# Performance work log

Hardware: AMD Instinct MI355X
Metric: run time of the kernel (lower is better)

The kernel has to match this reference:

```python
import jax, jax.numpy as jnp
import numpy as np

MODEL_DIM = 2048
INNER_DIM = 512
NUM_HEADS = 16
FFN_DIM = 8192
MEM_TOKENS = 64
BATCH = 2
SEQ = 2048
EPS = 1e-6


def _rmsnorm(x, w):
    # norm = ||x|| / sqrt(d); out = w * x / (norm + eps)
    norm = jnp.linalg.norm(x, axis=-1, keepdims=True) / np.sqrt(x.shape[-1])
    return w * x / (norm + EPS)


def setup_inputs() -> dict:
    key = jax.random.key(0)
    names_shapes = [
        ("x", (BATCH, SEQ, MODEL_DIM)), ("memory", (BATCH, MEM_TOKENS, MODEL_DIM)),
        ("wq", (MODEL_DIM, MODEL_DIM)), ("wk", (MODEL_DIM, MODEL_DIM)),
        ("wv", (MODEL_DIM, MODEL_DIM)), ("wz", (MODEL_DIM, MODEL_DIM)),
        ("wg", (MODEL_DIM, MODEL_DIM)),
        ("md1", (MODEL_DIM, INNER_DIM)), ("md2", (INNER_DIM, MODEL_DIM)),
        ("mcw", (MODEL_DIM, MODEL_DIM)),
        ("awq", (MODEL_DIM, MODEL_DIM)), ("awk", (MODEL_DIM, MODEL_DIM)),
        ("awv", (MODEL_DIM, MODEL_DIM)), ("awo", (MODEL_DIM, MODEL_DIM)),
        ("f1", (MODEL_DIM, FFN_DIM)), ("f2", (FFN_DIM, MODEL_DIM)),
    ]
    keys = jax.random.split(key, len(names_shapes))
    inp = {}
    for (name, shape), k in zip(names_shapes, keys):
        scale = 1.0 if name in ("x", "memory") else 0.02
        inp[name] = jax.random.normal(k, shape, dtype=jnp.float32) * scale
    for name, dim in [("bq", MODEL_DIM), ("bk", MODEL_DIM), ("bv", MODEL_DIM),
                      ("bz", MODEL_DIM), ("bg", MODEL_DIM), ("mb1", INNER_DIM),
                      ("mb2", MODEL_DIM), ("mcb", MODEL_DIM), ("abq", MODEL_DIM),
                      ("abk", MODEL_DIM), ("abv", MODEL_DIM), ("abo", MODEL_DIM),
                      ("fb1", FFN_DIM), ("fb2", MODEL_DIM)]:
        inp[name] = jnp.zeros((dim,), dtype=jnp.float32)
    inp["n1w"] = jnp.ones((MODEL_DIM,), dtype=jnp.float32)
    inp["n2w"] = jnp.ones((MODEL_DIM,), dtype=jnp.float32)
    return inp


def reference(x, memory, wq, bq, wk, bk, wv, bv, wz, bz, wg, bg, n1w, n2w,
              md1, mb1, md2, mb2, mcw, mcb, awq, abq, awk, abk, awv, abv,
              awo, abo, f1, fb1, f2, fb2):
    B, S, D = x.shape
    H = NUM_HEADS
    dh = D // H

    # 1. projections on RMS-normed input
    xn = _rmsnorm(x, n1w)
    k_ = xn @ wk + bk
    v_ = xn @ wv + bv  # computed as in original (feeds attention path via h_t)
    z = xn @ wz + bz

    # MDI decay gamma: 2-layer decay net + context modulation, sigmoid
    gamma = jax.nn.sigmoid((jax.nn.gelu(z @ md1 + mb1) @ md2 + mb2)
                           + (k_ @ mcw + mcb))

    # 2. associative scan (exponential cumulative product) on contiguous reshape
    g4 = gamma.reshape(B, H, S, dh)  # faithful torch .view semantics
    cumprod = jnp.cumprod(g4, axis=2).reshape(B, S, D)

    # 3-4. core formula: h_t = z_t * sigmoid(W_g h_prev) + gamma * h_prev
    gate = jax.nn.sigmoid(x @ wg + bg)
    h_t = z * gate + gamma * x

    # 5. multi-memory attention: queries from h_t, keys/values from memory bank
    qa = (h_t @ awq + abq).reshape(B, S, H, dh)
    ka = (memory @ awk + abk).reshape(B, -1, H, dh)
    va = (memory @ awv + abv).reshape(B, -1, H, dh)
    scores = jnp.einsum('bshd,bmhd->bhsm', qa, ka) / np.sqrt(dh)
    attn = jax.nn.softmax(scores, axis=-1)
    ctx = jnp.einsum('bhsm,bmhd->bshd', attn, va).reshape(B, S, D)
    mem_context = ctx @ awo + abo

    # 6. residuals (dropout in eval mode = identity)
    x_residual = x + (h_t + mem_context)

    # 7. FFN + residual
    xn2 = _rmsnorm(x_residual, n2w)
    ffn_out = jax.nn.gelu(xn2 @ f1 + fb1) @ f2 + fb2
    output = x_residual + ffn_out
    return output, cumprod
```

## Files before the change

### kernel.cpp

```cpp
#include <hip/hip_runtime.h>
#include <stdint.h>
#include <stddef.h>


#define DEV __device__ __forceinline__

typedef __attribute__((ext_vector_type(8))) short bh8;
typedef __attribute__((ext_vector_type(4))) float f32x4;

typedef __attribute__((address_space(1))) uint32_t gu32;
typedef __attribute__((address_space(3))) uint32_t lu32;

DEV void async16(const void* g, void* l) {
  __builtin_amdgcn_global_load_lds((gu32*)g, (lu32*)l, 16, 0, 0);
}

DEV float b2f(short s) {
  union { float f; uint32_t u; } x;
  x.u = ((uint32_t)(uint16_t)s) << 16;
  return x.f;
}
DEV short f2b(float f) {
  uint32_t u = __float_as_uint(f);
  u += 0x7fffu + ((u >> 16) & 1u);
  return (short)(u >> 16);
}
DEV float sigmoid_f(float x) { return 1.f / (1.f + __expf(-x)); }
DEV float gelu_f(float x) {
  float y = 0.7978845608028654f * (x + 0.044715f * x * x * x);
  float t = 1.f - 2.f / (__expf(2.f * y) + 1.f);
  return 0.5f * x * (1.f + t);
}

template <int EPI>
DEV void epi_store(float v, size_t idx, void* Cv, const void* aux0, const void* aux1) {
  if constexpr (EPI == 0) {
    ((short*)Cv)[idx] = f2b(v);
  } else if constexpr (EPI == 1) {
    ((short*)Cv)[idx] = f2b(gelu_f(v));
  } else if constexpr (EPI == 2) {
    ((float*)Cv)[idx] = v;
  } else if constexpr (EPI == 3) {
    ((float*)Cv)[idx] = sigmoid_f(v + ((const float*)aux0)[idx]);
  } else if constexpr (EPI == 4) {
    ((float*)Cv)[idx] = v + ((const float*)aux0)[idx] + b2f(((const short*)aux1)[idx]);
  } else {
    ((float*)Cv)[idx] = v + ((const float*)aux0)[idx];
  }
}

template <int EPI>
__global__ __launch_bounds__(512) void gemm8_k(
    const short* __restrict__ A, const short* __restrict__ Bt,
    const float* __restrict__ bias, void* Cv,
    const void* aux0, const void* aux1, int M, int N, int K) {
  __shared__ __align__(16) short sL[3 * 24576];
  const int tid  = threadIdx.x;
  const int lane = tid & 63;
  const int wave = tid >> 6;
  const int q = lane >> 4;
  const int r = lane & 15;
  const int wm = wave >> 2;
  const int wn = wave & 3;

  const int nwg = gridDim.x * gridDim.y;
  int flat = blockIdx.y * gridDim.x + blockIdx.x;
  flat = (flat & 7) * (nwg >> 3) + (flat >> 3);
  const int bx = flat % gridDim.x;
  const int by = flat / gridDim.x;
  const int m0 = by * 128;
  const int n0 = bx * 256;

  const int srow = tid >> 3;
  const int sk8  = (tid & 7) ^ (srow & 7);
  const short* pA = A  + (size_t)(m0 + srow) * K + sk8 * 8;
  const short* pB = Bt + (size_t)(n0 + srow) * K + sk8 * 8;
  const size_t K64 = (size_t)64 * K;
  short* dA = &sL[tid * 8];
  short* dB = &sL[8192 + tid * 8];

#define STAGE_B(bi, t) do {                        \
    const short* s_ = pB + (size_t)(t) * 64;       \
    short* d_ = dB + (bi) * 24576;                 \
    async16(s_,           d_);                     \
    async16(s_ + K64,     d_ + 4096);              \
    async16(s_ + 2 * K64, d_ + 8192);              \
    async16(s_ + 3 * K64, d_ + 12288);             \
  } while (0)
#define STAGE_A(bi, t) do {                        \
    const short* s_ = pA + (size_t)(t) * 64;       \
    short* d_ = dA + (bi) * 24576;                 \
    async16(s_,       d_);                         \
    async16(s_ + K64, d_ + 4096);                  \
  } while (0)

  const int swz0 = (q ^ (r & 7)) * 8;
  const int swz1 = ((4 + q) ^ (r & 7)) * 8;
  const int aRow = (wm * 64 + r) * 64;
  const int bRow = 8192 + (wn * 64 + r) * 64;

  f32x4 acc[4][4] = {};
  const int NT = K >> 6;

  STAGE_B(0, 0); STAGE_A(0, 0);
  if (NT > 1) {
    STAGE_B(1, 1); STAGE_A(1, 1);
    asm volatile("s_waitcnt vmcnt(6)" ::: "memory");
  } else {
    asm volatile("s_waitcnt vmcnt(0)" ::: "memory");
  }
  __builtin_amdgcn_s_barrier();

  int cb = 0;
  for (int t = 0; t < NT; ++t) {
    const short* buf = &sL[cb * 24576];
    bh8 af[4][2], bf[4][2];
#pragma unroll
    for (int i = 0; i < 4; ++i) {
      af[i][0] = *(const bh8*)&buf[aRow + i * 1024 + swz0];
      af[i][1] = *(const bh8*)&buf[aRow + i * 1024 + swz1];
    }
#pragma unroll
    for (int j = 0; j < 4; ++j) {
      bf[j][0] = *(const bh8*)&buf[bRow + j * 1024 + swz0];
      bf[j][1] = *(const bh8*)&buf[bRow + j * 1024 + swz1];
    }
    if (t + 2 < NT) {
      const int pb = (cb == 0) ? 2 : cb - 1;
      STAGE_B(pb, t + 2);
      STAGE_A(pb, t + 2);
    }
#pragma unroll
    for (int kk = 0; kk < 2; ++kk)
#pragma unroll
      for (int i = 0; i < 4; ++i)
#pragma unroll
        for (int j = 0; j < 4; ++j)
          acc[i][j] = __builtin_amdgcn_mfma_f32_16x16x32_bf16(
              af[i][kk], bf[j][kk], acc[i][j], 0, 0, 0);
    if (t + 2 < NT) asm volatile("s_waitcnt vmcnt(6)" ::: "memory");
    else            asm volatile("s_waitcnt vmcnt(0)" ::: "memory");
    __builtin_amdgcn_s_barrier();
    cb = (cb == 2) ? 0 : cb + 1;
  }
#undef STAGE_A
#undef STAGE_B

#pragma unroll
  for (int j = 0; j < 4; ++j) {
    const int col = n0 + wn * 64 + j * 16 + r;
    const float bv = bias[col];
#pragma unroll
    for (int i = 0; i < 4; ++i) {
#pragma unroll
      for (int rr = 0; rr < 4; ++rr) {
        const int row = m0 + wm * 64 + i * 16 + q * 4 + rr;
        const size_t idx = (size_t)row * N + col;
        epi_store<EPI>(acc[i][j][rr] + bv, idx, Cv, aux0, aux1);
      }
    }
  }
}

__global__ __launch_bounds__(256) void transpose_k(const float* __restrict__ in,
                                                   short* __restrict__ out,
                                                   int R, int C) {
  __shared__ float t[64][68];
  const int tx = threadIdx.x, ty = threadIdx.y;
  const int c0 = blockIdx.x * 64, r0 = blockIdx.y * 64;
#pragma unroll
  for (int yy = 0; yy < 64; yy += 16) {
    const float4 v = *(const float4*)&in[(size_t)(r0 + ty + yy) * C + c0 + tx * 4];
    t[ty + yy][tx * 4 + 0] = v.x;
    t[ty + yy][tx * 4 + 1] = v.y;
    t[ty + yy][tx * 4 + 2] = v.z;
    t[ty + yy][tx * 4 + 3] = v.w;
  }
  __syncthreads();
#pragma unroll
  for (int yy = 0; yy < 64; yy += 16) {
    short4 v;
    v.x = f2b(t[tx * 4 + 0][ty + yy]);
    v.y = f2b(t[tx * 4 + 1][ty + yy]);
    v.z = f2b(t[tx * 4 + 2][ty + yy]);
    v.w = f2b(t[tx * 4 + 3][ty + yy]);
    *(short4*)&out[(size_t)(c0 + ty + yy) * R + r0 + tx * 4] = v;
  }
}

__global__ __launch_bounds__(256) void cvt_k(const float* __restrict__ in,
                                             short* __restrict__ out) {
  const size_t i = ((size_t)blockIdx.x * 256 + threadIdx.x) * 4;
  const float4 v = *(const float4*)(in + i);
  short4 o;
  o.x = f2b(v.x); o.y = f2b(v.y); o.z = f2b(v.z); o.w = f2b(v.w);
  *(short4*)(out + i) = o;
}

__global__ __launch_bounds__(256) void rmsnorm_k(const float* __restrict__ in,
                                                 const float* __restrict__ w,
                                                 short* __restrict__ out) {
  const int row = blockIdx.x;
  const int tid = threadIdx.x;
  const size_t base = (size_t)row * 2048;
  float v[8];
  const float* p = in + base + tid * 8;
#pragma unroll
  for (int i = 0; i < 8; ++i) v[i] = p[i];
  float ss = 0.f;
#pragma unroll
  for (int i = 0; i < 8; ++i) ss += v[i] * v[i];
  for (int off = 32; off; off >>= 1) ss += __shfl_down(ss, off);
  __shared__ float red[4];
  __shared__ float sscale;
  if ((tid & 63) == 0) red[tid >> 6] = ss;
  __syncthreads();
  if (tid == 0) {
    float tot = red[0] + red[1] + red[2] + red[3];
    sscale = 1.f / (sqrtf(tot * (1.f / 2048.f)) + 1e-6f);
  }
  __syncthreads();
  const float scale = sscale;
  short* o = out + base + tid * 8;
#pragma unroll
  for (int i = 0; i < 8; ++i) o[i] = f2b(w[tid * 8 + i] * v[i] * scale);
}

__global__ __launch_bounds__(256) void ht_k(const short* __restrict__ z,
                                            const short* __restrict__ gp,
                                            const float* __restrict__ gamma,
                                            const float* __restrict__ x,
                                            short* __restrict__ ht) {
  const size_t i = ((size_t)blockIdx.x * 256 + threadIdx.x) * 4;
  const short4 z4 = *(const short4*)(z + i);
  const short4 g4 = *(const short4*)(gp + i);
  const float4 x4 = *(const float4*)(x + i);
  const float4 gm = *(const float4*)(gamma + i);
  short4 o;
  o.x = f2b(b2f(z4.x) * sigmoid_f(b2f(g4.x)) + gm.x * x4.x);
  o.y = f2b(b2f(z4.y) * sigmoid_f(b2f(g4.y)) + gm.y * x4.y);
  o.z = f2b(b2f(z4.z) * sigmoid_f(b2f(g4.z)) + gm.z * x4.z);
  o.w = f2b(b2f(z4.w) * sigmoid_f(b2f(g4.w)) + gm.w * x4.w);
  *(short4*)(ht + i) = o;
}

__global__ __launch_bounds__(128) void cumprod1_k(float* __restrict__ gamma,
                                                  float* __restrict__ segprod) {
  const int bx = blockIdx.x;
  const int b = bx >> 7, h = (bx >> 3) & 15, seg = bx & 7;
  size_t base = (size_t)b * 4194304 + (size_t)h * 262144 + (size_t)seg * 256 * 128 + threadIdx.x;
  float acc = 1.f;
  for (int s = 0; s < 256; ++s) {
    acc *= gamma[base + (size_t)s * 128];
    gamma[base + (size_t)s * 128] = acc;
  }
  segprod[(size_t)bx * 128 + threadIdx.x] = acc;
}

__global__ __launch_bounds__(128) void cumprod2_k(const float* __restrict__ gamma,
                                                  const float* __restrict__ segprod,
                                                  float* __restrict__ out) {
  const int bx = blockIdx.x;
  const int b = bx >> 7, h = (bx >> 3) & 15, seg = bx & 7;
  size_t base = (size_t)b * 4194304 + (size_t)h * 262144 + (size_t)seg * 256 * 128 + threadIdx.x;
  float pre = 1.f;
  const size_t sp0 = (size_t)(bx & ~7) * 128 + threadIdx.x;
  for (int t = 0; t < seg; ++t) pre *= segprod[sp0 + (size_t)t * 128];
  for (int s = 0; s < 256; ++s)
    out[base + (size_t)s * 128] = gamma[base + (size_t)s * 128] * pre;
}

__global__ __launch_bounds__(512) void attn_k(const short* __restrict__ qa,
                                              const short* __restrict__ ka,
                                              const short* __restrict__ va,
                                              short* __restrict__ ctx) {
  __shared__ short sk[64][136];
  __shared__ short sv[64][136];
  __shared__ float sq[32][128];
  __shared__ float ss[32][64];
  const int tid = threadIdx.x;
  const int b = blockIdx.z, h = blockIdx.y;
  const int s0 = blockIdx.x * 32;
  const size_t hoff = (size_t)h * 128;
  for (int i = tid; i < 64 * 128; i += 512) {
    int m = i >> 7, d = i & 127;
    sk[m][d] = ka[((size_t)b * 64 + m) * 2048 + hoff + d];
    sv[m][d] = va[((size_t)b * 64 + m) * 2048 + hoff + d];
  }
  for (int i = tid; i < 32 * 128; i += 512) {
    int s = i >> 7, d = i & 127;
    sq[s][d] = b2f(qa[((size_t)b * 2048 + s0 + s) * 2048 + hoff + d]);
  }
  __syncthreads();
  const int g = tid >> 4;
  const int t = tid & 15;
  float sc[4];
#pragma unroll
  for (int mi = 0; mi < 4; ++mi) {
    const int m = mi * 16 + t;
    float a = 0.f;
    for (int d = 0; d < 128; ++d) a += sq[g][d] * b2f(sk[m][d]);
    sc[mi] = a * 0.08838834764831843f;
  }
  float mx = fmaxf(fmaxf(sc[0], sc[1]), fmaxf(sc[2], sc[3]));
#pragma unroll
  for (int off = 8; off; off >>= 1) mx = fmaxf(mx, __shfl_xor(mx, off, 16));
  float sum = 0.f;
#pragma unroll
  for (int mi = 0; mi < 4; ++mi) { sc[mi] = __expf(sc[mi] - mx); sum += sc[mi]; }
#pragma unroll
  for (int off = 8; off; off >>= 1) sum += __shfl_xor(sum, off, 16);
  const float inv = 1.f / sum;
#pragma unroll
  for (int mi = 0; mi < 4; ++mi) ss[g][mi * 16 + t] = sc[mi] * inv;
  __syncthreads();
  const int d0 = t * 8;
  float o[8] = {};
  for (int m = 0; m < 64; ++m) {
    const float wgt = ss[g][m];
#pragma unroll
    for (int i = 0; i < 8; ++i) o[i] += wgt * b2f(sv[m][d0 + i]);
  }
  short* op = ctx + ((size_t)b * 2048 + s0 + g) * 2048 + hoff + d0;
#pragma unroll
  for (int i = 0; i < 8; ++i) op[i] = f2b(o[i]);
}

extern "C" void kernel_launch(void* const* d_in, const int* in_sizes, int n_in,
                              void* d_out, int out_size, void* d_ws, size_t ws_size,
                              hipStream_t stream) {
  (void)in_sizes; (void)n_in; (void)out_size; (void)ws_size;
  const float* x   = (const float*)d_in[0];
  const float* mem = (const float*)d_in[1];
  const float* wk  = (const float*)d_in[3];
  const float* wz  = (const float*)d_in[5];
  const float* wg  = (const float*)d_in[6];
  const float* md1 = (const float*)d_in[7];
  const float* md2 = (const float*)d_in[8];
  const float* mcw = (const float*)d_in[9];
  const float* awq = (const float*)d_in[10];
  const float* awk = (const float*)d_in[11];
  const float* awv = (const float*)d_in[12];
  const float* awo = (const float*)d_in[13];
  const float* f1  = (const float*)d_in[14];
  const float* f2  = (const float*)d_in[15];
  const float* bk  = (const float*)d_in[17];
  const float* bz  = (const float*)d_in[19];
  const float* bg  = (const float*)d_in[20];
  const float* mb1 = (const float*)d_in[21];
  const float* mb2 = (const float*)d_in[22];
  const float* mcb = (const float*)d_in[23];
  const float* abq = (const float*)d_in[24];
  const float* abk = (const float*)d_in[25];
  const float* abv = (const float*)d_in[26];
  const float* abo = (const float*)d_in[27];
  const float* fb1 = (const float*)d_in[28];
  const float* fb2 = (const float*)d_in[29];
  const float* n1w = (const float*)d_in[30];
  const float* n2w = (const float*)d_in[31];

  char* W = (char*)d_ws;
  short* wkT  = (short*)(W + 0);
  short* wzT  = (short*)(W + 8388608);
  short* wgT  = (short*)(W + 16777216);
  short* mcwT = (short*)(W + 25165824);
  short* md1T = (short*)(W + 33554432);
  short* md2T = (short*)(W + 35651584);
  short* awqT = (short*)(W + 37748736);
  short* awkT = (short*)(W + 46137344);
  short* awvT = (short*)(W + 54525952);
  short* awoT = (short*)(W + 62914560);
  short* f1T  = (short*)(W + 71303168);
  short* f2T  = (short*)(W + 104857600);
  char*  big  = W + 138412032;
  short* xn   = (short*)(big + 0);
  short* kk   = (short*)(big + 16777216);
  short* z    = (short*)(big + 33554432);
  short* gpre = (short*)(big + 50331648);
  short* ctx  = kk;
  short* t2   = (short*)big;
  short* t1   = (short*)(W + 205520896);
  float* gamma = (float*)(W + 209715200);
  float* xres  = gamma;
  short* ht   = (short*)(W + 243269632);
  short* qa   = (short*)(W + 260046848);
  short* xn2  = qa;
  short* xb   = (short*)(W + 276824064);
  short* memb = (short*)(W + 293601280);
  short* ka   = (short*)(W + 294125568);
  short* va   = (short*)(W + 294649856);
  float* segprod = (float*)(W + 295174144);

  float* out0 = (float*)d_out;
  float* out1 = out0 + 8388608;

  const dim3 tb16(16, 16);
  transpose_k<<<dim3(32, 32), tb16, 0, stream>>>(wk, wkT, 2048, 2048);
  transpose_k<<<dim3(32, 32), tb16, 0, stream>>>(wz, wzT, 2048, 2048);
  transpose_k<<<dim3(32, 32), tb16, 0, stream>>>(wg, wgT, 2048, 2048);
  transpose_k<<<dim3(32, 32), tb16, 0, stream>>>(mcw, mcwT, 2048, 2048);
  transpose_k<<<dim3(8, 32), tb16, 0, stream>>>(md1, md1T, 2048, 512);
  transpose_k<<<dim3(32, 8), tb16, 0, stream>>>(md2, md2T, 512, 2048);
  transpose_k<<<dim3(32, 32), tb16, 0, stream>>>(awq, awqT, 2048, 2048);
  transpose_k<<<dim3(32, 32), tb16, 0, stream>>>(awk, awkT, 2048, 2048);
  transpose_k<<<dim3(32, 32), tb16, 0, stream>>>(awv, awvT, 2048, 2048);
  transpose_k<<<dim3(32, 32), tb16, 0, stream>>>(awo, awoT, 2048, 2048);
  transpose_k<<<dim3(128, 32), tb16, 0, stream>>>(f1, f1T, 2048, 8192);
  transpose_k<<<dim3(32, 128), tb16, 0, stream>>>(f2, f2T, 8192, 2048);

  cvt_k<<<8192, 256, 0, stream>>>(x, xb);
  cvt_k<<<256, 256, 0, stream>>>(mem, memb);
  rmsnorm_k<<<4096, 256, 0, stream>>>(x, n1w, xn);

  gemm8_k<0><<<dim3(8, 32), 512, 0, stream>>>(xn, wkT, bk, kk, nullptr, nullptr, 4096, 2048, 2048);
  gemm8_k<0><<<dim3(8, 32), 512, 0, stream>>>(xn, wzT, bz, z, nullptr, nullptr, 4096, 2048, 2048);
  gemm8_k<0><<<dim3(8, 32), 512, 0, stream>>>(xb, wgT, bg, gpre, nullptr, nullptr, 4096, 2048, 2048);

  gemm8_k<1><<<dim3(2, 32), 512, 0, stream>>>(z, md1T, mb1, t1, nullptr, nullptr, 4096, 512, 2048);
  gemm8_k<2><<<dim3(8, 32), 512, 0, stream>>>(t1, md2T, mb2, gamma, nullptr, nullptr, 4096, 2048, 512);
  gemm8_k<3><<<dim3(8, 32), 512, 0, stream>>>(kk, mcwT, mcb, gamma, gamma, nullptr, 4096, 2048, 2048);

  ht_k<<<8192, 256, 0, stream>>>(z, gpre, gamma, x, ht);

  cumprod1_k<<<256, 128, 0, stream>>>(gamma, segprod);
  cumprod2_k<<<256, 128, 0, stream>>>(gamma, segprod, out1);

  gemm8_k<0><<<dim3(8, 32), 512, 0, stream>>>(ht, awqT, abq, qa, nullptr, nullptr, 4096, 2048, 2048);
  gemm8_k<0><<<dim3(8, 1), 512, 0, stream>>>(memb, awkT, abk, ka, nullptr, nullptr, 128, 2048, 2048);
  gemm8_k<0><<<dim3(8, 1), 512, 0, stream>>>(memb, awvT, abv, va, nullptr, nullptr, 128, 2048, 2048);

  attn_k<<<dim3(64, 16, 2), 512, 0, stream>>>(qa, ka, va, ctx);

  gemm8_k<4><<<dim3(8, 32), 512, 0, stream>>>(ctx, awoT, abo, xres, x, ht, 4096, 2048, 2048);

  rmsnorm_k<<<4096, 256, 0, stream>>>(xres, n2w, xn2);

  gemm8_k<1><<<dim3(32, 32), 512, 0, stream>>>(xn2, f1T, fb1, t2, nullptr, nullptr, 4096, 8192, 2048);
  gemm8_k<5><<<dim3(8, 32), 512, 0, stream>>>(t2, f2T, fb2, out0, xres, nullptr, 4096, 2048, 8192);
}
```

Before: 1.207 ms.

## Split GEMM k-step into barrier-separated halves and fuse h_t and x casts

The GEMM main loop is split into two half-k phases. Each phase loads its LDS fragments, issues part of the next prefetch, synchronises with a barrier and raises wave priority around its MFMA block, aiming to overlap LDS reads, global prefetch and matrix work across waves. The separate h_t elementwise kernel is folded into the gamma GEMM epilogue (new EPI 6), which writes h_t at a fixed offset from the gamma buffer. The bf16 cast of x is folded into the first RMSNorm kernel. Together these cut kernel launches and memory round-trips, at the cost of extra barriers per k-step and a hardcoded buffer-adjacency assumption for h_t.

```diff
diff --git a/kernel.cpp b/kernel.cpp
--- a/kernel.cpp
+++ b/kernel.cpp
@@ -33,7 +33,8 @@
 }
 
 template <int EPI>
-DEV void epi_store(float v, size_t idx, void* Cv, const void* aux0, const void* aux1) {
+DEV void epi_store(float v, size_t idx, void* Cv, const void* aux0,
+                   const void* aux1, const void* aux2, const void* aux3) {
   if constexpr (EPI == 0) {
     ((short*)Cv)[idx] = f2b(v);
   } else if constexpr (EPI == 1) {
@@ -44,8 +45,16 @@
     ((float*)Cv)[idx] = sigmoid_f(v + ((const float*)aux0)[idx]);
   } else if constexpr (EPI == 4) {
     ((float*)Cv)[idx] = v + ((const float*)aux0)[idx] + b2f(((const short*)aux1)[idx]);
+  } else if constexpr (EPI == 5) {
+    ((float*)Cv)[idx] = v + ((const float*)aux0)[idx];
   } else {
-    ((float*)Cv)[idx] = v + ((const float*)aux0)[idx];
+    const float g = sigmoid_f(v + ((const float*)aux0)[idx]);
+    ((float*)Cv)[idx] = g;
+    const float xv = ((const float*)aux1)[idx];
+    const float zz = b2f(((const short*)aux2)[idx]);
+    const float gp = b2f(((const short*)aux3)[idx]);
+    short* ht = (short*)((float*)Cv + 8388608);
+    ht[idx] = f2b(zz * sigmoid_f(gp) + g * xv);
   }
 }
 
@@ -53,7 +62,8 @@
 __global__ __launch_bounds__(512) void gemm8_k(
     const short* __restrict__ A, const short* __restrict__ Bt,
     const float* __restrict__ bias, void* Cv,
-    const void* aux0, const void* aux1, int M, int N, int K) {
+    const void* aux0, const void* aux1, const void* aux2, const void* aux3,
+    int M, int N, int K) {
   __shared__ __align__(16) short sL[3 * 24576];
   const int tid  = threadIdx.x;
   const int lane = tid & 63;
@@ -103,43 +113,55 @@
   const int NT = K >> 6;
 
   STAGE_B(0, 0); STAGE_A(0, 0);
-  if (NT > 1) {
-    STAGE_B(1, 1); STAGE_A(1, 1);
-    asm volatile("s_waitcnt vmcnt(6)" ::: "memory");
-  } else {
-    asm volatile("s_waitcnt vmcnt(0)" ::: "memory");
-  }
+  STAGE_B(1, 1); STAGE_A(1, 1);
+  asm volatile("s_waitcnt vmcnt(6)" ::: "memory");
   __builtin_amdgcn_s_barrier();
 
   int cb = 0;
   for (int t = 0; t < NT; ++t) {
     const short* buf = &sL[cb * 24576];
-    bh8 af[4][2], bf[4][2];
-#pragma unroll
-    for (int i = 0; i < 4; ++i) {
-      af[i][0] = *(const bh8*)&buf[aRow + i * 1024 + swz0];
-      af[i][1] = *(const bh8*)&buf[aRow + i * 1024 + swz1];
-    }
-#pragma unroll
-    for (int j = 0; j < 4; ++j) {
-      bf[j][0] = *(const bh8*)&buf[bRow + j * 1024 + swz0];
-      bf[j][1] = *(const bh8*)&buf[bRow + j * 1024 + swz1];
-    }
-    if (t + 2 < NT) {
-      const int pb = (cb == 0) ? 2 : cb - 1;
-      STAGE_B(pb, t + 2);
-      STAGE_A(pb, t + 2);
-    }
-#pragma unroll
-    for (int kk = 0; kk < 2; ++kk)
-#pragma unroll
-      for (int i = 0; i < 4; ++i)
-#pragma unroll
-        for (int j = 0; j < 4; ++j)
-          acc[i][j] = __builtin_amdgcn_mfma_f32_16x16x32_bf16(
-              af[i][kk], bf[j][kk], acc[i][j], 0, 0, 0);
-    if (t + 2 < NT) asm volatile("s_waitcnt vmcnt(6)" ::: "memory");
-    else            asm volatile("s_waitcnt vmcnt(0)" ::: "memory");
+    const int pb = (cb == 0) ? 2 : cb - 1;
+    const bool pf = (t + 2 < NT);
+
+    bh8 af0[4], bf0[4];
+#pragma unroll
+    for (int i = 0; i < 4; ++i) af0[i] = *(const bh8*)&buf[aRow + i * 1024 + swz0];
+#pragma unroll
+    for (int j = 0; j < 4; ++j) bf0[j] = *(const bh8*)&buf[bRow + j * 1024 + swz0];
+    if (pf) STAGE_B(pb, t + 2);
+    __builtin_amdgcn_s_barrier();
+    asm volatile("s_waitcnt lgkmcnt(0)" ::: "memory");
+    __builtin_amdgcn_sched_barrier(0);
+    __builtin_amdgcn_s_setprio(1);
+#pragma unroll
+    for (int i = 0; i < 4; ++i)
+#pragma unroll
+      for (int j = 0; j < 4; ++j)
+        acc[i][j] = __builtin_amdgcn_mfma_f32_16x16x32_bf16(
+            af0[i], bf0[j], acc[i][j], 0, 0, 0);
+    __builtin_amdgcn_s_setprio(0);
+    __builtin_amdgcn_s_barrier();
+
+    bh8 af1[4], bf1[4];
+#pragma unroll
+    for (int i = 0; i < 4; ++i) af1[i] = *(const bh8*)&buf[aRow + i * 1024 + swz1];
+#pragma unroll
+    for (int j = 0; j < 4; ++j) bf1[j] = *(const bh8*)&buf[bRow + j * 1024 + swz1];
+    if (pf) STAGE_A(pb, t + 2);
+    __builtin_amdgcn_s_barrier();
+    asm volatile("s_waitcnt lgkmcnt(0)" ::: "memory");
+    __builtin_amdgcn_sched_barrier(0);
+    __builtin_amdgcn_s_setprio(1);
+#pragma unroll
+    for (int i = 0; i < 4; ++i)
+#pragma unroll
+      for (int j = 0; j < 4; ++j)
+        acc[i][j] = __builtin_amdgcn_mfma_f32_16x16x32_bf16(
+            af1[i], bf1[j], acc[i][j], 0, 0, 0);
+    __builtin_amdgcn_s_setprio(0);
+
+    if (pf) asm volatile("s_waitcnt vmcnt(6)" ::: "memory");
+    else    asm volatile("s_waitcnt vmcnt(0)" ::: "memory");
     __builtin_amdgcn_s_barrier();
     cb = (cb == 2) ? 0 : cb + 1;
   }
@@ -156,7 +178,7 @@
       for (int rr = 0; rr < 4; ++rr) {
         const int row = m0 + wm * 64 + i * 16 + q * 4 + rr;
         const size_t idx = (size_t)row * N + col;
-        epi_store<EPI>(acc[i][j][rr] + bv, idx, Cv, aux0, aux1);
+        epi_store<EPI>(acc[i][j][rr] + bv, idx, Cv, aux0, aux1, aux2, aux3);
       }
     }
   }
@@ -199,7 +221,8 @@
 
 __global__ __launch_bounds__(256) void rmsnorm_k(const float* __restrict__ in,
                                                  const float* __restrict__ w,
-                                                 short* __restrict__ out) {
+                                                 short* __restrict__ out,
+                                                 short* __restrict__ xbout) {
   const int row = blockIdx.x;
   const int tid = threadIdx.x;
   const size_t base = (size_t)row * 2048;
@@ -207,6 +230,11 @@
   const float* p = in + base + tid * 8;
 #pragma unroll
   for (int i = 0; i < 8; ++i) v[i] = p[i];
+  if (xbout) {
+    short* xo = xbout + base + tid * 8;
+#pragma unroll
+    for (int i = 0; i < 8; ++i) xo[i] = f2b(v[i]);
+  }
   float ss = 0.f;
 #pragma unroll
   for (int i = 0; i < 8; ++i) ss += v[i] * v[i];
@@ -224,24 +252,6 @@
   short* o = out + base + tid * 8;
 #pragma unroll
   for (int i = 0; i < 8; ++i) o[i] = f2b(w[tid * 8 + i] * v[i] * scale);
-}
-
-__global__ __launch_bounds__(256) void ht_k(const short* __restrict__ z,
-                                            const short* __restrict__ gp,
-                                            const float* __restrict__ gamma,
-                                            const float* __restrict__ x,
-                                            short* __restrict__ ht) {
-  const size_t i = ((size_t)blockIdx.x * 256 + threadIdx.x) * 4;
-  const short4 z4 = *(const short4*)(z + i);
-  const short4 g4 = *(const short4*)(gp + i);
-  const float4 x4 = *(const float4*)(x + i);
-  const float4 gm = *(const float4*)(gamma + i);
-  short4 o;
-  o.x = f2b(b2f(z4.x) * sigmoid_f(b2f(g4.x)) + gm.x * x4.x);
-  o.y = f2b(b2f(z4.y) * sigmoid_f(b2f(g4.y)) + gm.y * x4.y);
-  o.z = f2b(b2f(z4.z) * sigmoid_f(b2f(g4.z)) + gm.z * x4.z);
-  o.w = f2b(b2f(z4.w) * sigmoid_f(b2f(g4.w)) + gm.w * x4.w);
-  *(short4*)(ht + i) = o;
 }
 
 __global__ __launch_bounds__(128) void cumprod1_k(float* __restrict__ gamma,
@@ -408,33 +418,30 @@
   transpose_k<<<dim3(128, 32), tb16, 0, stream>>>(f1, f1T, 2048, 8192);
   transpose_k<<<dim3(32, 128), tb16, 0, stream>>>(f2, f2T, 8192, 2048);
 
-  cvt_k<<<8192, 256, 0, stream>>>(x, xb);
   cvt_k<<<256, 256, 0, stream>>>(mem, memb);
-  rmsnorm_k<<<4096, 256, 0, stream>>>(x, n1w, xn);
-
-  gemm8_k<0><<<dim3(8, 32), 512, 0, stream>>>(xn, wkT, bk, kk, nullptr, nullptr, 4096, 2048, 2048);
-  gemm8_k<0><<<dim3(8, 32), 512, 0, stream>>>(xn, wzT, bz, z, nullptr, nullptr, 4096, 2048, 2048);
-  gemm8_k<0><<<dim3(8, 32), 512, 0, stream>>>(xb, wgT, bg, gpre, nullptr, nullptr, 4096, 2048, 2048);
-
-  gemm8_k<1><<<dim3(2, 32), 512, 0, stream>>>(z, md1T, mb1, t1, nullptr, nullptr, 4096, 512, 2048);
-  gemm8_k<2><<<dim3(8, 32), 512, 0, stream>>>(t1, md2T, mb2, gamma, nullptr, nullptr, 4096, 2048, 512);
-  gemm8_k<3><<<dim3(8, 32), 512, 0, stream>>>(kk, mcwT, mcb, gamma, gamma, nullptr, 4096, 2048, 2048);
-
-  ht_k<<<8192, 256, 0, stream>>>(z, gpre, gamma, x, ht);
+  rmsnorm_k<<<4096, 256, 0, stream>>>(x, n1w, xn, xb);
+
+  gemm8_k<0><<<dim3(8, 32), 512, 0, stream>>>(xn, wkT, bk, kk, nullptr, nullptr, nullptr, nullptr, 4096, 2048, 2048);
+  gemm8_k<0><<<dim3(8, 32), 512, 0, stream>>>(xn, wzT, bz, z, nullptr, nullptr, nullptr, nullptr, 4096, 2048, 2048);
+  gemm8_k<0><<<dim3(8, 32), 512, 0, stream>>>(xb, wgT, bg, gpre, nullptr, nullptr, nullptr, nullptr, 4096, 2048, 2048);
+
+  gemm8_k<1><<<dim3(2, 32), 512, 0, stream>>>(z, md1T, mb1, t1, nullptr, nullptr, nullptr, nullptr, 4096, 512, 2048);
+  gemm8_k<2><<<dim3(8, 32), 512, 0, stream>>>(t1, md2T, mb2, gamma, nullptr, nullptr, nullptr, nullptr, 4096, 2048, 512);
+  gemm8_k<6><<<dim3(8, 32), 512, 0, stream>>>(kk, mcwT, mcb, gamma, gamma, x, z, gpre, 4096, 2048, 2048);
 
   cumprod1_k<<<256, 128, 0, stream>>>(gamma, segprod);
   cumprod2_k<<<256, 128, 0, stream>>>(gamma, segprod, out1);
 
-  gemm8_k<0><<<dim3(8, 32), 512, 0, stream>>>(ht, awqT, abq, qa, nullptr, nullptr, 4096, 2048, 2048);
-  gemm8_k<0><<<dim3(8, 1), 512, 0, stream>>>(memb, awkT, abk, ka, nullptr, nullptr, 128, 2048, 2048);
-  gemm8_k<0><<<dim3(8, 1), 512, 0, stream>>>(memb, awvT, abv, va, nullptr, nullptr, 128, 2048, 2048);
+  gemm8_k<0><<<dim3(8, 32), 512, 0, stream>>>(ht, awqT, abq, qa, nullptr, nullptr, nullptr, nullptr, 4096, 2048, 2048);
+  gemm8_k<0><<<dim3(8, 1), 512, 0, stream>>>(memb, awkT, abk, ka, nullptr, nullptr, nullptr, nullptr, 128, 2048, 2048);
+  gemm8_k<0><<<dim3(8, 1), 512, 0, stream>>>(memb, awvT, abv, va, nullptr, nullptr, nullptr, nullptr, 128, 2048, 2048);
 
   attn_k<<<dim3(64, 16, 2), 512, 0, stream>>>(qa, ka, va, ctx);
 
-  gemm8_k<4><<<dim3(8, 32), 512, 0, stream>>>(ctx, awoT, abo, xres, x, ht, 4096, 2048, 2048);
-
-  rmsnorm_k<<<4096, 256, 0, stream>>>(xres, n2w, xn2);
-
-  gemm8_k<1><<<dim3(32, 32), 512, 0, stream>>>(xn2, f1T, fb1, t2, nullptr, nullptr, 4096, 8192, 2048);
-  gemm8_k<5><<<dim3(8, 32), 512, 0, stream>>>(t2, f2T, fb2, out0, xres, nullptr, 4096, 2048, 8192);
-}
+  gemm8_k<4><<<dim3(8, 32), 512, 0, stream>>>(ctx, awoT, abo, xres, x, ht, nullptr, nullptr, 4096, 2048, 2048);
+
+  rmsnorm_k<<<4096, 256, 0, stream>>>(xres, n2w, xn2, nullptr);
+
+  gemm8_k<1><<<dim3(32, 32), 512, 0, stream>>>(xn2, f1T, fb1, t2, nullptr, nullptr, nullptr, nullptr, 4096, 8192, 2048);
+  gemm8_k<5><<<dim3(8, 32), 512, 0, stream>>>(t2, f2T, fb2, out0, xres, nullptr, nullptr, nullptr, 4096, 2048, 8192);
+}
```

Result: slower. 1.257 ms (+4.1%).
